# Performance work log

Hardware: AMD Instinct MI355X
Metric: run time of the kernel (lower is better)

The kernel has to match this reference:

```python
import jax, jax.numpy as jnp
import numpy as np

N_NODES = 50000
N_EDGES = 800000
N_GRAPHS = 64
D_IN = 768
D_HID = 256


def gcn_conv(x, src, dst, W, b, n_nodes):
    """PyG GCNConv: symmetric-normalized aggregation with self-loops.
    out = D^{-1/2} (A + I) D^{-1/2} (x @ W) + b
    """
    h = x @ W  # [N, C_out]
    # degree from target nodes, counting the implicit self-loop (+1)
    deg = jax.ops.segment_sum(jnp.ones((src.shape[0],), h.dtype), dst,
                              num_segments=n_nodes) + 1.0
    dinv = jax.lax.rsqrt(deg)  # deg >= 1 always (self-loop)
    norm = (dinv[src] * dinv[dst])[:, None]  # [E, 1]
    agg = jax.ops.segment_sum(h[src] * norm, dst, num_segments=n_nodes)
    # self-loop contribution: norm_ii = dinv_i^2
    agg = agg + (dinv * dinv)[:, None] * h
    return agg + b


def global_mean_pool(x, batch, n_graphs):
    s = jax.ops.segment_sum(x, batch, num_segments=n_graphs)
    cnt = jax.ops.segment_sum(jnp.ones((x.shape[0],), x.dtype), batch,
                              num_segments=n_graphs)
    return s / jnp.maximum(cnt, 1.0)[:, None]


def setup_inputs() -> dict:
    key = jax.random.key(0)
    ks = jax.random.split(key, 12)
    x = jax.random.normal(ks[0], (N_NODES, D_IN), jnp.float32)
    edge_index = jax.random.randint(ks[1], (2, N_EDGES), 0, N_NODES, jnp.int64)
    batch = jnp.sort(jax.random.randint(ks[2], (N_NODES,), 0, N_GRAPHS, jnp.int64))
    def glorot(k, shape):
        lim = np.sqrt(6.0 / (shape[0] + shape[1]))
        return jax.random.uniform(k, shape, jnp.float32, -lim, lim)
    return {
        "x": x, "edge_index": edge_index, "batch": batch,
        "W1": glorot(ks[3], (D_IN, D_HID)), "b1": jnp.zeros((D_HID,), jnp.float32),
        "W2": glorot(ks[4], (D_HID, D_HID)), "b2": jnp.zeros((D_HID,), jnp.float32),
        "W3": glorot(ks[5], (D_HID, D_HID)), "b3": jnp.zeros((D_HID,), jnp.float32),
        "Wl": glorot(ks[6], (D_HID, D_IN)), "bl": jnp.zeros((D_IN,), jnp.float32),
    }


def reference(x, edge_index, batch, W1, b1, W2, b2, W3, b3, Wl, bl):
    src, dst = edge_index[0], edge_index[1]
    n = x.shape[0]
    # dropout is identity in eval mode
    h = jax.nn.relu(gcn_conv(x, src, dst, W1, b1, n))
    h = jax.nn.relu(gcn_conv(h, src, dst, W2, b2, n))
    h = gcn_conv(h, src, dst, W3, b3, n)
    g = global_mean_pool(h, batch, N_GRAPHS)  # [G, D_HID]
    return g @ Wl + bl  # [G, D_IN]
```

## Files before the change

kernel.cpp:

```cpp
#include <hip/hip_runtime.h>
#include <hip/hip_bf16.h>

#define D_IN 768
#define D_HID 256

typedef __attribute__((ext_vector_type(8))) short short8;
typedef __attribute__((ext_vector_type(4))) float f32x4;

__device__ inline float b2f(unsigned short u) {
    unsigned x = ((unsigned)u) << 16;
    union { unsigned u; float f; } c; c.u = x; return c.f;
}
__device__ inline unsigned short f2b(float v) {
    __hip_bfloat16 h = __float2bfloat16(v);
    return *(unsigned short*)&h;
}

__device__ inline void gload_lds16(const void* g, void* l) {
    __builtin_amdgcn_global_load_lds(
        (const __attribute__((address_space(1))) unsigned int*)g,
        (__attribute__((address_space(3))) unsigned int*)l, 16, 0, 0);
}


__global__ void k_count(const int* __restrict__ dst, int* __restrict__ deg, int E) {
    int i = blockIdx.x * 256 + threadIdx.x;
    if (i < E) atomicAdd(&deg[dst[i]], 1);
}

__global__ void k_dinv(const int* __restrict__ deg, float* __restrict__ dinv, int N) {
    int i = blockIdx.x * 256 + threadIdx.x;
    if (i < N) dinv[i] = rsqrtf((float)deg[i] + 1.0f);
}

__global__ __launch_bounds__(1024) void k_scan(const int* __restrict__ deg,
                                               int* __restrict__ row_ptr, int N) {
    __shared__ int wsum[16];
    __shared__ int carry_s;
    int t = threadIdx.x;
    int lane = t & 63, wid = t >> 6;
    if (t == 0) carry_s = 0;
    __syncthreads();
    for (int base = 0; base < N; base += 1024) {
        int i = base + t;
        int v = (i < N) ? deg[i] : 0;
        int s = v;
        #pragma unroll
        for (int d = 1; d < 64; d <<= 1) {
            int tmp = __shfl_up(s, d);
            if (lane >= d) s += tmp;
        }
        if (lane == 63) wsum[wid] = s;
        __syncthreads();
        if (wid == 0 && lane < 16) {
            int ws = wsum[lane];
            #pragma unroll
            for (int d = 1; d < 16; d <<= 1) {
                int tmp = __shfl_up(ws, d);
                if (lane >= d) ws += tmp;
            }
            wsum[lane] = ws;
        }
        __syncthreads();
        int carry = carry_s;
        int woff = (wid > 0) ? wsum[wid - 1] : 0;
        if (i < N) row_ptr[i] = carry + woff + s - v;
        __syncthreads();
        if (t == 0) carry_s = carry + wsum[15];
        __syncthreads();
    }
    if (t == 0) row_ptr[N] = carry_s;
}

__global__ void k_fill(const int* __restrict__ src, const int* __restrict__ dst,
                       const int* __restrict__ row_ptr, int* __restrict__ wptr,
                       int* __restrict__ csr_src, int E) {
    int i = blockIdx.x * 256 + threadIdx.x;
    if (i < E) {
        int d = dst[i];
        int w = atomicAdd(&wptr[d], 1);
        csr_src[row_ptr[d] + w] = src[i];
    }
}

__global__ void k_bounds(const int* __restrict__ batch, int* __restrict__ cnt,
                         int* __restrict__ offg, int N, int G) {
    int g = threadIdx.x;
    if (g >= G) return;
    auto lower = [&](int key) {
        int lo = 0, hi = N;
        while (lo < hi) {
            int mid = (lo + hi) >> 1;
            if (batch[mid] < key) lo = mid + 1; else hi = mid;
        }
        return lo;
    };
    int lo = lower(g);
    int hi = lower(g + 1);
    offg[g] = lo;
    cnt[g] = hi - lo;
}

__global__ __launch_bounds__(256) void k_wc(const float* __restrict__ W3,
                                            const float* __restrict__ Wl,
                                            float* __restrict__ Wc) {
    __shared__ float w3s[16][256];
    int t = threadIdx.x;
    int cx = blockIdx.x, iq = blockIdx.y;
    #pragma unroll
    for (int r = 0; r < 16; ++r)
        w3s[r][t] = W3[(size_t)(iq * 16 + r) * 256 + t];
    __syncthreads();
    int c = cx * 256 + t;
    float acc[16];
    #pragma unroll
    for (int i = 0; i < 16; ++i) acc[i] = 0.f;
    for (int m = 0; m < 256; ++m) {
        float wl = Wl[(size_t)m * 768 + c];
        #pragma unroll
        for (int i = 0; i < 16; ++i) acc[i] = fmaf(w3s[i][m], wl, acc[i]);
    }
    #pragma unroll
    for (int i = 0; i < 16; ++i)
        Wc[(size_t)(iq * 16 + i) * 768 + c] = acc[i];
}

__global__ __launch_bounds__(256) void k_bc(const float* __restrict__ b3,
                                            const float* __restrict__ Wl,
                                            const float* __restrict__ bl,
                                            float* __restrict__ bc) {
    __shared__ float b3s[256];
    int t = threadIdx.x;
    b3s[t] = b3[t];
    __syncthreads();
    int c = blockIdx.x * 256 + t;
    float acc = bl[c];
    for (int m = 0; m < 256; ++m) acc = fmaf(b3s[m], Wl[(size_t)m * 768 + c], acc);
    bc[c] = acc;
}

__global__ void k_prep_B(const float* __restrict__ W, short* __restrict__ Bp, int KA) {
    int t = blockIdx.x * 256 + threadIdx.x;
    if (t >= KA * 256) return;
    int k = t >> 8, n = t & 255;
    float v = W[(size_t)k * 256 + n];
    unsigned short h = f2b(v);
    unsigned short l = f2b(v - b2f(h));
    int c = k >> 5, q = (k >> 3) & 3, j = k & 7;
    int tile = n >> 4, ln = n & 15;
    size_t base = (size_t)c * 16384 + (size_t)(tile * 4 + q) * 128 + ln * 8 + j;
    Bp[base] = (short)h;
    Bp[base + 8192] = (short)l;
}

template <int MODE>
__global__ __launch_bounds__(512, 4) void k_gemm6(const void* __restrict__ Av,
                                                  const short* __restrict__ Bp,
                                                  unsigned short* __restrict__ C,
                                                  int M) {
    constexpr int KA = (MODE == 1) ? D_IN : D_HID;
    constexpr int NCH = KA / 32;
    __shared__ short Bs[2][16384];

    int t = threadIdx.x;
    int lane = t & 63, w = t >> 6;
    int wr = w >> 2, wc = w & 3;
    int ln = lane & 15, q = lane >> 4;
    int bm = blockIdx.x * 64;

    const char* Abase[2];
    #pragma unroll
    for (int s = 0; s < 2; ++s) {
        int rr = bm + wr * 32 + s * 16 + ln;
        rr = (rr < M) ? rr : (M - 1);
        Abase[s] = (const char*)Av + (size_t)rr * KA * ((MODE == 1) ? 4 : 2);
    }

    f32x4 acc[2][4];
    #pragma unroll
    for (int s = 0; s < 2; ++s)
        #pragma unroll
        for (int tt = 0; tt < 4; ++tt) acc[s][tt] = (f32x4){0.f, 0.f, 0.f, 0.f};

    auto stage = [&](int c, int pb) {
        #pragma unroll
        for (int i = 0; i < 4; ++i) {
            int seg = i * 8 + w;
            gload_lds16(Bp + (size_t)c * 16384 + seg * 512 + lane * 8,
                        &Bs[pb][seg * 512]);
        }
    };

    stage(0, 0);

    f32x4 cur0[2], cur1[2];
    short8 curb[2];
    #pragma unroll
    for (int s = 0; s < 2; ++s) {
        if (MODE == 1) {
            const float* Af = (const float*)(Abase[s]) + q * 8;
            cur0[s] = *(const f32x4*)Af;
            cur1[s] = *(const f32x4*)(Af + 4);
        } else {
            curb[s] = *(const short8*)((const unsigned short*)(Abase[s]) + q * 8);
        }
    }
    __syncthreads();

    for (int c = 0; c < NCH; ++c) {
        int pb = c & 1;
        bool more = (c + 1 < NCH);
        if (more) stage(c + 1, pb ^ 1);

        f32x4 nxt0[2], nxt1[2];
        short8 nxtb[2];
        if (more) {
            #pragma unroll
            for (int s = 0; s < 2; ++s) {
                if (MODE == 1) {
                    const float* Af = (const float*)(Abase[s]) + (c + 1) * 32 + q * 8;
                    nxt0[s] = *(const f32x4*)Af;
                    nxt1[s] = *(const f32x4*)(Af + 4);
                } else {
                    nxtb[s] = *(const short8*)((const unsigned short*)(Abase[s]) + (c + 1) * 32 + q * 8);
                }
            }
        }

        short8 a_hi[2], a_lo[2];
        #pragma unroll
        for (int s = 0; s < 2; ++s) {
            if (MODE == 1) {
                float vv[8] = {cur0[s][0], cur0[s][1], cur0[s][2], cur0[s][3],
                               cur1[s][0], cur1[s][1], cur1[s][2], cur1[s][3]};
                #pragma unroll
                for (int j = 0; j < 8; ++j) {
                    unsigned short h = f2b(vv[j]);
                    a_hi[s][j] = (short)h;
                    a_lo[s][j] = (short)f2b(vv[j] - b2f(h));
                }
            } else {
                a_hi[s] = curb[s];
            }
        }

        #pragma unroll
        for (int tt = 0; tt < 4; ++tt) {
            int T = wc * 4 + tt;
            const short* bp = &Bs[pb][(size_t)(T * 4 + q) * 128 + ln * 8];
            short8 bh = *(const short8*)bp;
            short8 bl2 = *(const short8*)(bp + 8192);
            #pragma unroll
            for (int s = 0; s < 2; ++s) {
                acc[s][tt] = __builtin_amdgcn_mfma_f32_16x16x32_bf16(a_hi[s], bh, acc[s][tt], 0, 0, 0);
                if (MODE == 1)
                    acc[s][tt] = __builtin_amdgcn_mfma_f32_16x16x32_bf16(a_lo[s], bh, acc[s][tt], 0, 0, 0);
                acc[s][tt] = __builtin_amdgcn_mfma_f32_16x16x32_bf16(a_hi[s], bl2, acc[s][tt], 0, 0, 0);
            }
        }
        __syncthreads();

        if (more) {
            #pragma unroll
            for (int s = 0; s < 2; ++s) {
                if (MODE == 1) { cur0[s] = nxt0[s]; cur1[s] = nxt1[s]; }
                else           { curb[s] = nxtb[s]; }
            }
        }
    }

    #pragma unroll
    for (int s = 0; s < 2; ++s)
        #pragma unroll
        for (int tt = 0; tt < 4; ++tt)
            #pragma unroll
            for (int r = 0; r < 4; ++r) {
                int row = bm + wr * 32 + s * 16 + q * 4 + r;
                if (row < M)
                    C[(size_t)row * 256 + wc * 64 + tt * 16 + ln] = f2b(acc[s][tt][r]);
            }
}

template <int RELU, int OUTBF>
__global__ __launch_bounds__(256) void k_agg(const unsigned short* __restrict__ hin,
                                             void* __restrict__ hout,
                                             const int* __restrict__ row_ptr,
                                             const int* __restrict__ csr_src,
                                             const float* __restrict__ dinv,
                                             const float* __restrict__ bias, int N) {
    int w = threadIdx.x >> 6;
    int lane = threadIdx.x & 63;
    int row = blockIdx.x * 4 + w;
    if (row >= N) return;
    int half = lane >> 5;
    int hl = lane & 31;
    int c8 = hl * 8;

    int2 se = *(const int2*)&row_ptr[row];
    int s = se.x, e = se.y;

    float di = dinv[row];
    short8 vs = *(const short8*)&hin[(size_t)row * 256 + c8];
    float4 bb0 = *(const float4*)&bias[c8];
    float4 bb1 = *(const float4*)&bias[c8 + 4];

    float acc[8];
    #pragma unroll
    for (int ch = 0; ch < 8; ++ch) acc[ch] = 0.f;

    int j = s;
    for (; j + 8 <= e; j += 8) {
        int u[4];
        float dv[4];
        short8 v[4];
        #pragma unroll
        for (int p = 0; p < 4; ++p) {
            int2 uu = *(const int2*)&csr_src[j + 2 * p];
            u[p] = half ? uu.y : uu.x;
        }
        #pragma unroll
        for (int p = 0; p < 4; ++p) dv[p] = dinv[u[p]];
        #pragma unroll
        for (int p = 0; p < 4; ++p) v[p] = *(const short8*)&hin[(size_t)u[p] * 256 + c8];
        #pragma unroll
        for (int p = 0; p < 4; ++p)
            #pragma unroll
            for (int ch = 0; ch < 8; ++ch)
                acc[ch] += dv[p] * b2f((unsigned short)v[p][ch]);
    }
    for (; j + 2 <= e; j += 2) {
        int2 uu = *(const int2*)&csr_src[j];
        int u = half ? uu.y : uu.x;
        float dv = dinv[u];
        short8 v = *(const short8*)&hin[(size_t)u * 256 + c8];
        #pragma unroll
        for (int ch = 0; ch < 8; ++ch) acc[ch] += dv * b2f((unsigned short)v[ch]);
    }
    if (j < e) {
        int u = csr_src[j];
        float dv = half ? 0.f : dinv[u];
        short8 v = *(const short8*)&hin[(size_t)u * 256 + c8];
        #pragma unroll
        for (int ch = 0; ch < 8; ++ch) acc[ch] += dv * b2f((unsigned short)v[ch]);
    }

    #pragma unroll
    for (int ch = 0; ch < 8; ++ch) acc[ch] += __shfl_xor(acc[ch], 32);

    float dii = di * di;
    float r[8];
    #pragma unroll
    for (int ch = 0; ch < 8; ++ch) {
        float b = (ch < 4) ? ((ch == 0) ? bb0.x : (ch == 1) ? bb0.y : (ch == 2) ? bb0.z : bb0.w)
                           : ((ch == 4) ? bb1.x : (ch == 5) ? bb1.y : (ch == 6) ? bb1.z : bb1.w);
        r[ch] = acc[ch] * di + dii * b2f((unsigned short)vs[ch]) + b;
        if (RELU) r[ch] = fmaxf(r[ch], 0.f);
    }

    float r0 = half ? r[4] : r[0];
    float r1 = half ? r[5] : r[1];
    float r2 = half ? r[6] : r[2];
    float r3 = half ? r[7] : r[3];
    int cofs = c8 + half * 4;

    if (OUTBF) {
        ushort4 o;
        o.x = f2b(r0); o.y = f2b(r1); o.z = f2b(r2); o.w = f2b(r3);
        *(ushort4*)((unsigned short*)hout + (size_t)row * 256 + cofs) = o;
    } else {
        *(float4*)((float*)hout + (size_t)row * 256 + cofs) = make_float4(r0, r1, r2, r3);
    }
}

__global__ __launch_bounds__(256) void k_pool(const float* __restrict__ h,
                                              const int* __restrict__ cnt,
                                              const int* __restrict__ offg,
                                              float* __restrict__ g) {
    int gi = blockIdx.x, slice = blockIdx.y;
    int c = threadIdx.x;
    int start = offg[gi], n = cnt[gi];
    int per = (n + (int)gridDim.y - 1) / (int)gridDim.y;
    int r0 = slice * per;
    int r1 = min(n, r0 + per);
    float acc = 0.f;
    for (int r = r0; r < r1; ++r) acc += h[(size_t)(start + r) * D_HID + c];
    if (r1 > r0) atomicAdd(&g[gi * D_HID + c], acc);
}

__global__ __launch_bounds__(256) void k_final(const float* __restrict__ g,
                                               const int* __restrict__ cnt,
                                               const float* __restrict__ Wc,
                                               const float* __restrict__ bc,
                                               float* __restrict__ out) {
    __shared__ float gs[D_HID];
    int t = threadIdx.x;
    int gi = blockIdx.y;
    int c = blockIdx.x * 256 + t;
    float inv = 1.0f / (float)max(cnt[gi], 1);
    gs[t] = g[gi * D_HID + t] * inv;
    __syncthreads();
    float acc = bc[c];
    #pragma unroll 8
    for (int k = 0; k < D_HID; ++k) acc = fmaf(gs[k], Wc[(size_t)k * D_IN + c], acc);
    out[(size_t)gi * D_IN + c] = acc;
}


extern "C" void kernel_launch(void* const* d_in, const int* in_sizes, int n_in,
                              void* d_out, int out_size, void* d_ws, size_t ws_size,
                              hipStream_t stream) {
    const float* x     = (const float*)d_in[0];
    const int*   ei    = (const int*)d_in[1];
    const int*   batch = (const int*)d_in[2];
    const float* W1 = (const float*)d_in[3];
    const float* b1 = (const float*)d_in[4];
    const float* W2 = (const float*)d_in[5];
    const float* b2 = (const float*)d_in[6];
    const float* W3 = (const float*)d_in[7];
    const float* b3 = (const float*)d_in[8];
    const float* Wl = (const float*)d_in[9];
    const float* bl = (const float*)d_in[10];
    float* out = (float*)d_out;

    int N = in_sizes[2];
    int E = in_sizes[1] / 2;
    int G = out_size / D_IN;
    const int* srcp = ei;
    const int* dstp = ei + E;

    char* ws = (char*)d_ws;
    size_t o = 0;
    auto alloc = [&](size_t bytes) -> char* {
        char* p = ws + o;
        o += (bytes + 255) & ~(size_t)255;
        return p;
    };
    int*   deg     = (int*)alloc((size_t)N * 4);
    int*   wptr    = (int*)alloc((size_t)N * 4);
    int*   row_ptr = (int*)alloc((size_t)(N + 1) * 4);
    int*   cnt     = (int*)alloc((size_t)G * 4);
    int*   offg    = (int*)alloc((size_t)G * 4);
    int*   csr_src = (int*)alloc((size_t)E * 4);
    float* dinv    = (float*)alloc((size_t)N * 4);
    float* gbuf    = (float*)alloc((size_t)G * D_HID * 4);
    float* zbias   = (float*)alloc((size_t)D_HID * 4);
    float* Wc      = (float*)alloc((size_t)D_HID * D_IN * 4);
    float* bc      = (float*)alloc((size_t)D_IN * 4);
    unsigned short* hG  = (unsigned short*)alloc((size_t)N * D_HID * 2);
    unsigned short* hA2 = (unsigned short*)alloc((size_t)N * D_HID * 2);
    float* hF      = (float*)alloc((size_t)N * D_HID * 4);
    short* Bp1     = (short*)alloc((size_t)(D_IN / 32) * 16384 * 2);
    short* Bp2     = (short*)alloc((size_t)(D_HID / 32) * 16384 * 2);

    hipMemsetAsync(deg, 0, (size_t)N * 4, stream);
    hipMemsetAsync(wptr, 0, (size_t)N * 4, stream);
    hipMemsetAsync(gbuf, 0, (size_t)G * D_HID * 4, stream);
    hipMemsetAsync(zbias, 0, (size_t)D_HID * 4, stream);

    int gE = (E + 255) / 256;
    int gN = (N + 255) / 256;

    k_count<<<gE, 256, 0, stream>>>(dstp, deg, E);
    k_dinv<<<gN, 256, 0, stream>>>(deg, dinv, N);
    k_scan<<<1, 1024, 0, stream>>>(deg, row_ptr, N);
    k_fill<<<gE, 256, 0, stream>>>(srcp, dstp, row_ptr, wptr, csr_src, E);
    k_bounds<<<1, 64, 0, stream>>>(batch, cnt, offg, N, G);

    k_prep_B<<<D_IN, 256, 0, stream>>>(W1, Bp1, D_IN);
    k_prep_B<<<D_HID, 256, 0, stream>>>(W2, Bp2, D_HID);
    dim3 wc_grid(3, 16);
    k_wc<<<wc_grid, 256, 0, stream>>>(W3, Wl, Wc);
    k_bc<<<3, 256, 0, stream>>>(b3, Wl, bl, bc);

    int gemm_grid = (N + 63) / 64;
    int agg_grid = (N + 3) / 4;

    k_gemm6<1><<<gemm_grid, 512, 0, stream>>>(x, Bp1, hG, N);
    k_agg<1, 1><<<agg_grid, 256, 0, stream>>>(hG, hA2, row_ptr, csr_src, dinv, b1, N);
    k_gemm6<2><<<gemm_grid, 512, 0, stream>>>(hA2, Bp2, hG, N);
    k_agg<1, 1><<<agg_grid, 256, 0, stream>>>(hG, hA2, row_ptr, csr_src, dinv, b2, N);
    k_agg<0, 0><<<agg_grid, 256, 0, stream>>>(hA2, hF, row_ptr, csr_src, dinv, zbias, N);

    dim3 pool_grid(G, 8);
    k_pool<<<pool_grid, 256, 0, stream>>>(hF, cnt, offg, gbuf);
    dim3 fin_grid(D_IN / 256, G);
    k_final<<<fin_grid, 256, 0, stream>>>(gbuf, cnt, Wc, bc, out);
}
```

Baseline: 765.0 us.

## Retile GEMM to 128x128 blocks and batch edge-index loads in aggregation

The GEMM now gives each block a 128-row by 128-column tile, with a 2-wide grid over output columns. This halves the B tile staged in shared memory per block, lowers LDS use and doubles the rows that share each staged B chunk. The aggregation kernel now loads up to 64 neighbor indices and their dinv values cooperatively, one per lane, and passes them to the other lanes with shuffles instead of issuing a scalar load per edge. The cost is that each A row is read by two column blocks, and the aggregation adds shuffle overhead.

```diff
diff --git a/kernel.cpp b/kernel.cpp
--- a/kernel.cpp
+++ b/kernel.cpp
@@ -154,24 +154,26 @@
 }
 
 template <int MODE>
-__global__ __launch_bounds__(512, 4) void k_gemm6(const void* __restrict__ Av,
+__global__ __launch_bounds__(512, 4) void k_gemm7(const void* __restrict__ Av,
                                                   const short* __restrict__ Bp,
                                                   unsigned short* __restrict__ C,
                                                   int M) {
     constexpr int KA = (MODE == 1) ? D_IN : D_HID;
     constexpr int NCH = KA / 32;
-    __shared__ short Bs[2][16384];
+    __shared__ short Bs[2][8192];
 
     int t = threadIdx.x;
     int lane = t & 63, w = t >> 6;
-    int wr = w >> 2, wc = w & 3;
+    int wr2 = w >> 1, wc2 = w & 1;
     int ln = lane & 15, q = lane >> 4;
-    int bm = blockIdx.x * 64;
+    int bm = blockIdx.x * 128;
+    int bn = blockIdx.y * 128;
+    int TB = blockIdx.y * 8;
 
     const char* Abase[2];
     #pragma unroll
     for (int s = 0; s < 2; ++s) {
-        int rr = bm + wr * 32 + s * 16 + ln;
+        int rr = bm + wr2 * 32 + s * 16 + ln;
         rr = (rr < M) ? rr : (M - 1);
         Abase[s] = (const char*)Av + (size_t)rr * KA * ((MODE == 1) ? 4 : 2);
     }
@@ -183,12 +185,10 @@
         for (int tt = 0; tt < 4; ++tt) acc[s][tt] = (f32x4){0.f, 0.f, 0.f, 0.f};
 
     auto stage = [&](int c, int pb) {
-        #pragma unroll
-        for (int i = 0; i < 4; ++i) {
-            int seg = i * 8 + w;
-            gload_lds16(Bp + (size_t)c * 16384 + seg * 512 + lane * 8,
-                        &Bs[pb][seg * 512]);
-        }
+        gload_lds16(Bp + (size_t)c * 16384 + (size_t)(TB + w) * 512 + lane * 8,
+                    &Bs[pb][w * 512]);
+        gload_lds16(Bp + (size_t)c * 16384 + 8192 + (size_t)(TB + w) * 512 + lane * 8,
+                    &Bs[pb][4096 + w * 512]);
     };
 
     stage(0, 0);
@@ -246,10 +246,9 @@
 
         #pragma unroll
         for (int tt = 0; tt < 4; ++tt) {
-            int T = wc * 4 + tt;
-            const short* bp = &Bs[pb][(size_t)(T * 4 + q) * 128 + ln * 8];
+            const short* bp = &Bs[pb][(size_t)(wc2 * 4 + tt) * 512 + q * 128 + ln * 8];
             short8 bh = *(const short8*)bp;
-            short8 bl2 = *(const short8*)(bp + 8192);
+            short8 bl2 = *(const short8*)(bp + 4096);
             #pragma unroll
             for (int s = 0; s < 2; ++s) {
                 acc[s][tt] = __builtin_amdgcn_mfma_f32_16x16x32_bf16(a_hi[s], bh, acc[s][tt], 0, 0, 0);
@@ -275,9 +274,9 @@
         for (int tt = 0; tt < 4; ++tt)
             #pragma unroll
             for (int r = 0; r < 4; ++r) {
-                int row = bm + wr * 32 + s * 16 + q * 4 + r;
+                int row = bm + wr2 * 32 + s * 16 + q * 4 + r;
                 if (row < M)
-                    C[(size_t)row * 256 + wc * 64 + tt * 16 + ln] = f2b(acc[s][tt][r]);
+                    C[(size_t)row * 256 + bn + wc2 * 64 + tt * 16 + ln] = f2b(acc[s][tt][r]);
             }
 }
 
@@ -308,40 +307,46 @@
     #pragma unroll
     for (int ch = 0; ch < 8; ++ch) acc[ch] = 0.f;
 
-    int j = s;
-    for (; j + 8 <= e; j += 8) {
-        int u[4];
-        float dv[4];
-        short8 v[4];
-        #pragma unroll
-        for (int p = 0; p < 4; ++p) {
-            int2 uu = *(const int2*)&csr_src[j + 2 * p];
-            u[p] = half ? uu.y : uu.x;
-        }
-        #pragma unroll
-        for (int p = 0; p < 4; ++p) dv[p] = dinv[u[p]];
-        #pragma unroll
-        for (int p = 0; p < 4; ++p) v[p] = *(const short8*)&hin[(size_t)u[p] * 256 + c8];
-        #pragma unroll
-        for (int p = 0; p < 4; ++p)
-            #pragma unroll
-            for (int ch = 0; ch < 8; ++ch)
-                acc[ch] += dv[p] * b2f((unsigned short)v[p][ch]);
-    }
-    for (; j + 2 <= e; j += 2) {
-        int2 uu = *(const int2*)&csr_src[j];
-        int u = half ? uu.y : uu.x;
-        float dv = dinv[u];
-        short8 v = *(const short8*)&hin[(size_t)u * 256 + c8];
-        #pragma unroll
-        for (int ch = 0; ch < 8; ++ch) acc[ch] += dv * b2f((unsigned short)v[ch]);
-    }
-    if (j < e) {
-        int u = csr_src[j];
-        float dv = half ? 0.f : dinv[u];
-        short8 v = *(const short8*)&hin[(size_t)u * 256 + c8];
-        #pragma unroll
-        for (int ch = 0; ch < 8; ++ch) acc[ch] += dv * b2f((unsigned short)v[ch]);
+    for (int base = s; base < e; base += 64) {
+        int cnt = e - base;
+        if (cnt > 64) cnt = 64;
+        int gidx = base + lane;
+        if (gidx >= e) gidx = e - 1;
+        int myu = csr_src[gidx];
+        float mydv = dinv[myu];
+
+        int p = 0;
+        for (; p + 8 <= cnt; p += 8) {
+            int u[4];
+            float dv[4];
+            short8 v[4];
+            #pragma unroll
+            for (int qq = 0; qq < 4; ++qq) {
+                u[qq]  = __shfl(myu,  p + 2 * qq + half);
+                dv[qq] = __shfl(mydv, p + 2 * qq + half);
+            }
+            #pragma unroll
+            for (int qq = 0; qq < 4; ++qq) v[qq] = *(const short8*)&hin[(size_t)u[qq] * 256 + c8];
+            #pragma unroll
+            for (int qq = 0; qq < 4; ++qq)
+                #pragma unroll
+                for (int ch = 0; ch < 8; ++ch)
+                    acc[ch] += dv[qq] * b2f((unsigned short)v[qq][ch]);
+        }
+        for (; p + 2 <= cnt; p += 2) {
+            int u  = __shfl(myu,  p + half);
+            float dv = __shfl(mydv, p + half);
+            short8 v = *(const short8*)&hin[(size_t)u * 256 + c8];
+            #pragma unroll
+            for (int ch = 0; ch < 8; ++ch) acc[ch] += dv * b2f((unsigned short)v[ch]);
+        }
+        if (p < cnt) {
+            int u = __shfl(myu, p);
+            float dv = half ? 0.f : __shfl(mydv, p);
+            short8 v = *(const short8*)&hin[(size_t)u * 256 + c8];
+            #pragma unroll
+            for (int ch = 0; ch < 8; ++ch) acc[ch] += dv * b2f((unsigned short)v[ch]);
+        }
     }
 
     #pragma unroll
@@ -472,12 +477,12 @@
     k_wc<<<wc_grid, 256, 0, stream>>>(W3, Wl, Wc);
     k_bc<<<3, 256, 0, stream>>>(b3, Wl, bl, bc);
 
-    int gemm_grid = (N + 63) / 64;
+    dim3 gemm_grid((N + 127) / 128, 2);
     int agg_grid = (N + 3) / 4;
 
-    k_gemm6<1><<<gemm_grid, 512, 0, stream>>>(x, Bp1, hG, N);
+    k_gemm7<1><<<gemm_grid, 512, 0, stream>>>(x, Bp1, hG, N);
     k_agg<1, 1><<<agg_grid, 256, 0, stream>>>(hG, hA2, row_ptr, csr_src, dinv, b1, N);
-    k_gemm6<2><<<gemm_grid, 512, 0, stream>>>(hA2, Bp2, hG, N);
+    k_gemm7<2><<<gemm_grid, 512, 0, stream>>>(hA2, Bp2, hG, N);
     k_agg<1, 1><<<agg_grid, 256, 0, stream>>>(hG, hA2, row_ptr, csr_src, dinv, b2, N);
     k_agg<0, 0><<<agg_grid, 256, 0, stream>>>(hA2, hF, row_ptr, csr_src, dinv, zbias, N);
 
```

New measurement: 753.6 us. Within noise of the previous version (-1.5%).
